# Performance work log

Hardware: AMD Instinct MI355X
Metric: run time of the kernel (lower is better)

Reference implementation:

```python
import jax, jax.numpy as jnp
import numpy as np

P = 2              # partition_size
L = 16             # n_levels
F = 2              # n_features_per_level
LOG2_T = 19
T = 1 << LOG2_T    # hashmap size per level
BASE_RES = 16.0
PER_LEVEL_SCALE = 1.5
N_POINTS = 2_000_000
N_PART = P ** 3    # 8 encoders

# 8 corner offsets of a voxel, bit d of corner c
_CORNERS = np.array([[(c >> d) & 1 for d in range(3)] for c in range(8)])
CORNERS_U = jnp.asarray(_CORNERS, dtype=jnp.uint32)          # [8,3]
CORNERS_B = jnp.asarray(_CORNERS.astype(bool))               # [8,3]
PRIMES = jnp.array([1, 2654435761, 805459861], dtype=jnp.uint32)


def setup_inputs() -> dict:
    key = jax.random.key(0)
    k1, k2 = jax.random.split(key)
    coords = jax.random.uniform(k1, (N_POINTS, 3), dtype=jnp.float32)
    # one hash table per partition encoder, stacked: [8, L, T, F], init U(-1e-4, 1e-4)
    tables = jax.random.uniform(k2, (N_PART, L, T, F), dtype=jnp.float32,
                                minval=-1e-4, maxval=1e-4)
    return {"coords": coords, "tables": tables}


def _hash_grid_encode(coords, tables, flat_idx):
    # coords: [N,3] in [0,1]; tables: [8,L,T,F]; flat_idx: [N] partition id per point.
    outs = []
    for l in range(L):
        res = float(np.floor(BASE_RES * PER_LEVEL_SCALE ** l))
        scaled = coords * res                                   # [N,3]
        f0 = jnp.floor(scaled)
        frac = scaled - f0                                      # [N,3]
        corner = f0.astype(jnp.uint32)[:, None, :] + CORNERS_U[None]   # [N,8,3]
        h = (corner[..., 0] * PRIMES[0]) ^ (corner[..., 1] * PRIMES[1]) \
            ^ (corner[..., 2] * PRIMES[2])
        h = (h & jnp.uint32(T - 1)).astype(jnp.int32)           # [N,8]
        emb = tables[flat_idx[:, None], l, h]                   # [N,8,F] gather
        # trilinear weights: prod over dims of frac (corner bit=1) or 1-frac (bit=0)
        w = jnp.prod(jnp.where(CORNERS_B[None], frac[:, None, :],
                               1.0 - frac[:, None, :]), axis=-1)  # [N,8]
        outs.append(jnp.sum(w[..., None] * emb, axis=1))        # [N,F]
    return jnp.concatenate(outs, axis=-1)                       # [N, L*F]


def reference(coords, tables):
    coords = coords.astype(jnp.float32)
    # partition routing (torch does this under no_grad)
    cell = jnp.clip(jnp.floor(coords * P).astype(jnp.int32), 0, P - 1)  # [N,3]
    flat_idx = cell[:, 0] * (P * P) + cell[:, 1] * P + cell[:, 2]       # [N]
    return _hash_grid_encode(coords, tables, flat_idx)                  # [N,32]
```

## Files before the change

kernel.cpp:

```cpp
#include <hip/hip_runtime.h>
#include <hip/hip_bf16.h>

#define N_POINTS 2000000
#define NLEV 16
#define LOG2_T 19
#define T_MASK ((1u << LOG2_T) - 1u)
#define TF ((size_t)(1u << LOG2_T) * 2)

#define PTS_PER_BLK 256
#define CHUNKS ((N_POINTS + PTS_PER_BLK - 1) / PTS_PER_BLK)

typedef float f32x2 __attribute__((ext_vector_type(2)));

__constant__ float c_res[NLEV] = {
    16.f, 24.f, 36.f, 54.f, 81.f, 121.f, 182.f, 273.f,
    410.f, 615.f, 922.f, 1383.f, 2075.f, 3113.f, 4670.f, 7006.f
};

__global__ __launch_bounds__(256) void hash_enc_lvlmajor(
        const float* __restrict__ coords,
        const float* __restrict__ tables,
        f32x2* __restrict__ ws) {
    const int b = blockIdx.x;
    const int l = b / CHUNKS;
    const int n = (b % CHUNKS) * PTS_PER_BLK + threadIdx.x;
    if (n >= N_POINTS) return;

    const float cx = coords[n * 3 + 0];
    const float cy = coords[n * 3 + 1];
    const float cz = coords[n * 3 + 2];

    int px = (int)floorf(cx * 2.0f); px = px < 0 ? 0 : (px > 1 ? 1 : px);
    int py = (int)floorf(cy * 2.0f); py = py < 0 ? 0 : (py > 1 ? 1 : py);
    int pz = (int)floorf(cz * 2.0f); pz = pz < 0 ? 0 : (pz > 1 ? 1 : pz);
    const int flat = px * 4 + py * 2 + pz;

    const float* __restrict__ tb = tables + ((size_t)(flat * NLEV + l)) * TF;

    const float res = c_res[l];
    const float sx = cx * res, sy = cy * res, sz = cz * res;
    const float fx0 = floorf(sx), fy0 = floorf(sy), fz0 = floorf(sz);
    const float fx = sx - fx0, fy = sy - fy0, fz = sz - fz0;

    const uint32_t ix = (uint32_t)fx0;
    const uint32_t iy = (uint32_t)fy0;
    const uint32_t iz = (uint32_t)fz0;

    const uint32_t hx0 = ix;
    const uint32_t hx1 = ix + 1u;
    const uint32_t hy0 = iy * 2654435761u;
    const uint32_t hy1 = (iy + 1u) * 2654435761u;
    const uint32_t hz0 = iz * 805459861u;
    const uint32_t hz1 = (iz + 1u) * 805459861u;

    const float gx = 1.0f - fx, gy = 1.0f - fy, gz = 1.0f - fz;

    float s0 = 0.0f, s1 = 0.0f;
    #pragma unroll
    for (int c = 0; c < 8; ++c) {
        const uint32_t h = (((c & 1) ? hx1 : hx0)
                          ^ ((c & 2) ? hy1 : hy0)
                          ^ ((c & 4) ? hz1 : hz0)) & T_MASK;
        const f32x2 e = *(const f32x2*)(tb + (size_t)h * 2);
        float w = ((c & 1) ? fx : gx) * ((c & 2) ? fy : gy);
        w = w * ((c & 4) ? fz : gz);
        s0 += w * e.x;
        s1 += w * e.y;
    }

    f32x2 r; r.x = s0; r.y = s1;
    __builtin_nontemporal_store(r, &ws[(size_t)l * N_POINTS + n]);
}

__global__ __launch_bounds__(256) void transpose_lvl_to_pt(
        const f32x2* __restrict__ ws,
        f32x2* __restrict__ out) {
    __shared__ f32x2 tile[NLEV][PTS_PER_BLK + 1];

    const int n0 = blockIdx.x * PTS_PER_BLK;
    const int t = threadIdx.x;

    #pragma unroll
    for (int l = 0; l < NLEV; ++l) {
        const int n = n0 + t;
        if (n < N_POINTS)
            tile[l][t] = __builtin_nontemporal_load(&ws[(size_t)l * N_POINTS + n]);
    }
    __syncthreads();

    const int ll = t & 15;
    const int hi = t >> 4;
    #pragma unroll
    for (int j = 0; j < NLEV; ++j) {
        const int pp = j * 16 + hi;
        const int n = n0 + pp;
        if (n < N_POINTS)
            __builtin_nontemporal_store(tile[ll][pp], &out[(size_t)n * NLEV + ll]);
    }
}

__global__ __launch_bounds__(256) void hash_enc_direct(
        const float* __restrict__ coords,
        const float* __restrict__ tables,
        float* __restrict__ out) {
    const int tid = blockIdx.x * blockDim.x + threadIdx.x;
    if (tid >= N_POINTS * NLEV) return;
    const int n = tid >> 4;
    const int l = tid & 15;

    const float cx = coords[n * 3 + 0];
    const float cy = coords[n * 3 + 1];
    const float cz = coords[n * 3 + 2];

    int px = (int)floorf(cx * 2.0f); px = px < 0 ? 0 : (px > 1 ? 1 : px);
    int py = (int)floorf(cy * 2.0f); py = py < 0 ? 0 : (py > 1 ? 1 : py);
    int pz = (int)floorf(cz * 2.0f); pz = pz < 0 ? 0 : (pz > 1 ? 1 : pz);
    const int flat = px * 4 + py * 2 + pz;

    const float* __restrict__ tb = tables + ((size_t)(flat * NLEV + l)) * TF;

    const float res = c_res[l];
    const float sx = cx * res, sy = cy * res, sz = cz * res;
    const float fx0 = floorf(sx), fy0 = floorf(sy), fz0 = floorf(sz);
    const float fx = sx - fx0, fy = sy - fy0, fz = sz - fz0;

    const uint32_t ix = (uint32_t)fx0;
    const uint32_t iy = (uint32_t)fy0;
    const uint32_t iz = (uint32_t)fz0;

    const uint32_t hx0 = ix, hx1 = ix + 1u;
    const uint32_t hy0 = iy * 2654435761u, hy1 = (iy + 1u) * 2654435761u;
    const uint32_t hz0 = iz * 805459861u,  hz1 = (iz + 1u) * 805459861u;

    const float gx = 1.0f - fx, gy = 1.0f - fy, gz = 1.0f - fz;

    float s0 = 0.0f, s1 = 0.0f;
    #pragma unroll
    for (int c = 0; c < 8; ++c) {
        const uint32_t h = (((c & 1) ? hx1 : hx0)
                          ^ ((c & 2) ? hy1 : hy0)
                          ^ ((c & 4) ? hz1 : hz0)) & T_MASK;
        const f32x2 e = *(const f32x2*)(tb + (size_t)h * 2);
        float w = ((c & 1) ? fx : gx) * ((c & 2) ? fy : gy);
        w = w * ((c & 4) ? fz : gz);
        s0 += w * e.x;
        s1 += w * e.y;
    }
    f32x2 r; r.x = s0; r.y = s1;
    ((f32x2*)out)[tid] = r;
}

extern "C" void kernel_launch(void* const* d_in, const int* in_sizes, int n_in,
                              void* d_out, int out_size, void* d_ws, size_t ws_size,
                              hipStream_t stream) {
    const float* coords = (const float*)d_in[0];
    const float* tables = (const float*)d_in[1];

    const size_t ws_needed = (size_t)N_POINTS * NLEV * sizeof(f32x2);

    if (ws_size >= ws_needed) {
        f32x2* ws = (f32x2*)d_ws;
        hash_enc_lvlmajor<<<NLEV * CHUNKS, 256, 0, stream>>>(coords, tables, ws);
        transpose_lvl_to_pt<<<CHUNKS, 256, 0, stream>>>(ws, (f32x2*)d_out);
    } else {
        const int total = N_POINTS * NLEV;
        hash_enc_direct<<<(total + 255) / 256, 256, 0, stream>>>(coords, tables, (float*)d_out);
    }
}
```

Baseline: 1.692 ms.

## Store intermediate level-major results as packed fp16 and process four points per thread

```diff
diff --git a/kernel.cpp b/kernel.cpp
--- a/kernel.cpp
+++ b/kernel.cpp
@@ -1,5 +1,5 @@
 #include <hip/hip_runtime.h>
-#include <hip/hip_bf16.h>
+#include <hip/hip_fp16.h>
 
 #define N_POINTS 2000000
 #define NLEV 16
@@ -9,53 +9,39 @@
 
 #define PTS_PER_BLK 256
 #define CHUNKS ((N_POINTS + PTS_PER_BLK - 1) / PTS_PER_BLK)
+#define NCH4 ((N_POINTS + 1023) / 1024)
 
 typedef float f32x2 __attribute__((ext_vector_type(2)));
+typedef float f32x4 __attribute__((ext_vector_type(4)));
+typedef unsigned u32;
+typedef u32 u32x4 __attribute__((ext_vector_type(4)));
 
 __constant__ float c_res[NLEV] = {
     16.f, 24.f, 36.f, 54.f, 81.f, 121.f, 182.f, 273.f,
     410.f, 615.f, 922.f, 1383.f, 2075.f, 3113.f, 4670.f, 7006.f
 };
 
-__global__ __launch_bounds__(256) void hash_enc_lvlmajor(
-        const float* __restrict__ coords,
-        const float* __restrict__ tables,
-        f32x2* __restrict__ ws) {
-    const int b = blockIdx.x;
-    const int l = b / CHUNKS;
-    const int n = (b % CHUNKS) * PTS_PER_BLK + threadIdx.x;
-    if (n >= N_POINTS) return;
+#define WSOUT_F16_BYTES ((size_t)NLEV * N_POINTS * 4)
 
-    const float cx = coords[n * 3 + 0];
-    const float cy = coords[n * 3 + 1];
-    const float cz = coords[n * 3 + 2];
-
+__device__ __forceinline__ int part_of(float cx, float cy, float cz) {
     int px = (int)floorf(cx * 2.0f); px = px < 0 ? 0 : (px > 1 ? 1 : px);
     int py = (int)floorf(cy * 2.0f); py = py < 0 ? 0 : (py > 1 ? 1 : py);
     int pz = (int)floorf(cz * 2.0f); pz = pz < 0 ? 0 : (pz > 1 ? 1 : pz);
-    const int flat = px * 4 + py * 2 + pz;
+    return px * 4 + py * 2 + pz;
+}
 
-    const float* __restrict__ tb = tables + ((size_t)(flat * NLEV + l)) * TF;
-
-    const float res = c_res[l];
+__device__ __forceinline__ void enc_core(
+        const float* __restrict__ tb, float res,
+        float cx, float cy, float cz, float& s0, float& s1) {
     const float sx = cx * res, sy = cy * res, sz = cz * res;
     const float fx0 = floorf(sx), fy0 = floorf(sy), fz0 = floorf(sz);
     const float fx = sx - fx0, fy = sy - fy0, fz = sz - fz0;
-
-    const uint32_t ix = (uint32_t)fx0;
-    const uint32_t iy = (uint32_t)fy0;
-    const uint32_t iz = (uint32_t)fz0;
-
-    const uint32_t hx0 = ix;
-    const uint32_t hx1 = ix + 1u;
-    const uint32_t hy0 = iy * 2654435761u;
-    const uint32_t hy1 = (iy + 1u) * 2654435761u;
-    const uint32_t hz0 = iz * 805459861u;
-    const uint32_t hz1 = (iz + 1u) * 805459861u;
-
+    const uint32_t ix = (uint32_t)fx0, iy = (uint32_t)fy0, iz = (uint32_t)fz0;
+    const uint32_t hx0 = ix, hx1 = ix + 1u;
+    const uint32_t hy0 = iy * 2654435761u, hy1 = (iy + 1u) * 2654435761u;
+    const uint32_t hz0 = iz * 805459861u,  hz1 = (iz + 1u) * 805459861u;
     const float gx = 1.0f - fx, gy = 1.0f - fy, gz = 1.0f - fz;
-
-    float s0 = 0.0f, s1 = 0.0f;
+    s0 = 0.0f; s1 = 0.0f;
     #pragma unroll
     for (int c = 0; c < 8; ++c) {
         const uint32_t h = (((c & 1) ? hx1 : hx0)
@@ -67,16 +53,47 @@
         s0 += w * e.x;
         s1 += w * e.y;
     }
-
-    f32x2 r; r.x = s0; r.y = s1;
-    __builtin_nontemporal_store(r, &ws[(size_t)l * N_POINTS + n]);
 }
 
-__global__ __launch_bounds__(256) void transpose_lvl_to_pt(
-        const f32x2* __restrict__ ws,
-        f32x2* __restrict__ out) {
-    __shared__ f32x2 tile[NLEV][PTS_PER_BLK + 1];
+__device__ __forceinline__ u32 pack_f16(float s0, float s1) {
+    return (u32)__half_as_ushort(__float2half(s0))
+         | ((u32)__half_as_ushort(__float2half(s1)) << 16);
+}
 
+__global__ __launch_bounds__(256) void enc4_k(
+        const float* __restrict__ coords,
+        const float* __restrict__ tables,
+        u32* __restrict__ wsout) {
+    const int b = blockIdx.x;
+    const int l = b / NCH4;
+    const int chunk = b - l * NCH4;
+    const int n = (chunk * 256 + threadIdx.x) * 4;
+    if (n >= N_POINTS) return;
+
+    const f32x4 c0 = *(const f32x4*)(coords + (size_t)n * 3 + 0);
+    const f32x4 c1 = *(const f32x4*)(coords + (size_t)n * 3 + 4);
+    const f32x4 c2 = *(const f32x4*)(coords + (size_t)n * 3 + 8);
+    const float X[4] = { c0.x, c0.w, c1.z, c2.y };
+    const float Y[4] = { c0.y, c1.x, c1.w, c2.z };
+    const float Z[4] = { c0.z, c1.y, c2.x, c2.w };
+
+    const float res = c_res[l];
+    u32x4 pk;
+    #pragma unroll
+    for (int k = 0; k < 4; ++k) {
+        const int part = part_of(X[k], Y[k], Z[k]);
+        const float* __restrict__ tb = tables + ((size_t)(part * NLEV + l)) * TF;
+        float s0, s1;
+        enc_core(tb, res, X[k], Y[k], Z[k], s0, s1);
+        pk[k] = pack_f16(s0, s1);
+    }
+
+    __builtin_nontemporal_store(pk, (u32x4*)&wsout[(size_t)l * N_POINTS + n]);
+}
+
+__global__ __launch_bounds__(256) void transpose_f16_k(
+        const u32* __restrict__ wsout, f32x2* __restrict__ out) {
+    __shared__ u32 tile[NLEV][PTS_PER_BLK + 1];
     const int n0 = blockIdx.x * PTS_PER_BLK;
     const int t = threadIdx.x;
 
@@ -84,7 +101,7 @@
     for (int l = 0; l < NLEV; ++l) {
         const int n = n0 + t;
         if (n < N_POINTS)
-            tile[l][t] = __builtin_nontemporal_load(&ws[(size_t)l * N_POINTS + n]);
+            tile[l][t] = __builtin_nontemporal_load(&wsout[(size_t)l * N_POINTS + n]);
     }
     __syncthreads();
 
@@ -94,8 +111,13 @@
     for (int j = 0; j < NLEV; ++j) {
         const int pp = j * 16 + hi;
         const int n = n0 + pp;
-        if (n < N_POINTS)
-            __builtin_nontemporal_store(tile[ll][pp], &out[(size_t)n * NLEV + ll]);
+        if (n < N_POINTS) {
+            const u32 w = tile[ll][pp];
+            f32x2 e;
+            e.x = __half2float(__ushort_as_half((unsigned short)(w & 0xFFFFu)));
+            e.y = __half2float(__ushort_as_half((unsigned short)(w >> 16)));
+            __builtin_nontemporal_store(e, &out[(size_t)n * NLEV + ll]);
+        }
     }
 }
 
@@ -107,47 +129,12 @@
     if (tid >= N_POINTS * NLEV) return;
     const int n = tid >> 4;
     const int l = tid & 15;
-
-    const float cx = coords[n * 3 + 0];
-    const float cy = coords[n * 3 + 1];
-    const float cz = coords[n * 3 + 2];
-
-    int px = (int)floorf(cx * 2.0f); px = px < 0 ? 0 : (px > 1 ? 1 : px);
-    int py = (int)floorf(cy * 2.0f); py = py < 0 ? 0 : (py > 1 ? 1 : py);
-    int pz = (int)floorf(cz * 2.0f); pz = pz < 0 ? 0 : (pz > 1 ? 1 : pz);
-    const int flat = px * 4 + py * 2 + pz;
-
-    const float* __restrict__ tb = tables + ((size_t)(flat * NLEV + l)) * TF;
-
-    const float res = c_res[l];
-    const float sx = cx * res, sy = cy * res, sz = cz * res;
-    const float fx0 = floorf(sx), fy0 = floorf(sy), fz0 = floorf(sz);
-    const float fx = sx - fx0, fy = sy - fy0, fz = sz - fz0;
-
-    const uint32_t ix = (uint32_t)fx0;
-    const uint32_t iy = (uint32_t)fy0;
-    const uint32_t iz = (uint32_t)fz0;
-
-    const uint32_t hx0 = ix, hx1 = ix + 1u;
-    const uint32_t hy0 = iy * 2654435761u, hy1 = (iy + 1u) * 2654435761u;
-    const uint32_t hz0 = iz * 805459861u,  hz1 = (iz + 1u) * 805459861u;
-
-    const float gx = 1.0f - fx, gy = 1.0f - fy, gz = 1.0f - fz;
-
-    float s0 = 0.0f, s1 = 0.0f;
-    #pragma unroll
-    for (int c = 0; c < 8; ++c) {
-        const uint32_t h = (((c & 1) ? hx1 : hx0)
-                          ^ ((c & 2) ? hy1 : hy0)
-                          ^ ((c & 4) ? hz1 : hz0)) & T_MASK;
-        const f32x2 e = *(const f32x2*)(tb + (size_t)h * 2);
-        float w = ((c & 1) ? fx : gx) * ((c & 2) ? fy : gy);
-        w = w * ((c & 4) ? fz : gz);
-        s0 += w * e.x;
-        s1 += w * e.y;
-    }
-    f32x2 r; r.x = s0; r.y = s1;
-    ((f32x2*)out)[tid] = r;
+    const float cx = coords[n*3+0], cy = coords[n*3+1], cz = coords[n*3+2];
+    const int flat = part_of(cx, cy, cz);
+    float s0, s1;
+    enc_core(tables + ((size_t)(flat * NLEV + l)) * TF, c_res[l], cx, cy, cz, s0, s1);
+    f32x2 rr; rr.x = s0; rr.y = s1;
+    ((f32x2*)out)[tid] = rr;
 }
 
 extern "C" void kernel_launch(void* const* d_in, const int* in_sizes, int n_in,
@@ -156,14 +143,13 @@
     const float* coords = (const float*)d_in[0];
     const float* tables = (const float*)d_in[1];
 
-    const size_t ws_needed = (size_t)N_POINTS * NLEV * sizeof(f32x2);
-
-    if (ws_size >= ws_needed) {
-        f32x2* ws = (f32x2*)d_ws;
-        hash_enc_lvlmajor<<<NLEV * CHUNKS, 256, 0, stream>>>(coords, tables, ws);
-        transpose_lvl_to_pt<<<CHUNKS, 256, 0, stream>>>(ws, (f32x2*)d_out);
+    if (ws_size >= WSOUT_F16_BYTES) {
+        u32* wsout = (u32*)d_ws;
+        enc4_k<<<NLEV * NCH4, 256, 0, stream>>>(coords, tables, wsout);
+        transpose_f16_k<<<CHUNKS, 256, 0, stream>>>(wsout, (f32x2*)d_out);
     } else {
         const int total = N_POINTS * NLEV;
-        hash_enc_direct<<<(total + 255) / 256, 256, 0, stream>>>(coords, tables, (float*)d_out);
+        hash_enc_direct<<<(total + 255) / 256, 256, 0, stream>>>(
+            coords, tables, (float*)d_out);
     }
 }
```

Result: slower. 1.941 ms (+14.8%).
